# Optimization experiments

Measured on AMD Instinct MI355X. Metric: run time of the kernel, lower is better.

Reference implementation:

```python
import jax, jax.numpy as jnp
import numpy as np

TOP_K = 6
N_EXPERTS = 64
ALPHA = 1e-3


def setup_inputs() -> dict:
    key = jax.random.key(0)
    k1, k2 = jax.random.split(key)
    bsz, seq_len, h = 4, 4096, 2048
    hidden_states = jax.random.normal(k1, (bsz, seq_len, h), dtype=jnp.float32)
    # kaiming_uniform_(a=sqrt(5)) on [E, h] -> bound = 1/sqrt(h)
    bound = 1.0 / np.sqrt(h)
    weight = jax.random.uniform(k2, (N_EXPERTS, h), dtype=jnp.float32, minval=-bound, maxval=bound)
    return {"hidden_states": hidden_states, "weight": weight}


def reference(hidden_states, weight):
    bsz, seq_len, h = hidden_states.shape
    E = weight.shape[0]
    x = hidden_states.reshape(-1, h)                      # [T, h], T = bsz*seq_len
    logits = jnp.einsum('th,eh->te', x, weight)           # router linear (no bias)
    scores = jax.nn.softmax(logits, axis=-1)              # [T, E]
    topk_weight, topk_idx = jax.lax.top_k(scores, TOP_K)  # [T, K]
    # norm_topk_prob renormalization
    topk_weight = topk_weight / (jnp.sum(topk_weight, axis=-1, keepdims=True) + 1e-20)
    # seq_aux auxiliary load-balancing loss (training path)
    idx_b = topk_idx.reshape(bsz, seq_len * TOP_K)        # [B, S*K]
    ce = jnp.sum(jax.nn.one_hot(idx_b, E, dtype=scores.dtype), axis=1)  # [B, E] counts
    ce = ce / (seq_len * TOP_K / E)
    mean_scores = scores.reshape(bsz, seq_len, E).mean(axis=1)          # [B, E]
    aux_loss = jnp.mean(jnp.sum(ce * mean_scores, axis=1)) * ALPHA
    return topk_idx, topk_weight, aux_loss
```

## Files before the change

### kernel.cpp

```cpp
#include <hip/hip_runtime.h>
#include <math.h>

#pragma clang fp contract(off)

typedef float f32x2 __attribute__((ext_vector_type(2)));

#define T_TOKENS 16384
#define HDIM 2048
#define NEXP 64
#define TOPK 6
#define SEQ 4096
#define TPB 32
#define NTHR 256
#define KC 64
#define WS 68
#define LGS 65

__global__ __launch_bounds__(NTHR, 4) void moe_gate_main(
    const float* __restrict__ x, const float* __restrict__ wgt,
    float* __restrict__ out, float* __restrict__ gacc)
{
    __shared__ float w_lds[NEXP * WS];
    __shared__ float lg[TPB * LGS];
    __shared__ float probs[TPB * LGS];
    __shared__ float psum[4 * NEXP];
    __shared__ int   cnt[NEXP];

    const int tid = threadIdx.x;
    const int bid = blockIdx.x;
    const int tb  = bid * TPB;
    const int b   = tb >> 12;

    const int le = tid & 15;
    const int h  = (tid >> 4) & 1;
    const int tg = tid >> 5;
    const int t0 = tg * 4;

    f32x2 acc[4][4];
    #pragma unroll
    for (int je = 0; je < 4; ++je)
        #pragma unroll
        for (int tt = 0; tt < 4; ++tt) { acc[je][tt].x = 0.f; acc[je][tt].y = 0.f; }

    const float* xb = x + (size_t)(tb + t0) * HDIM + 2 * h;

    for (int c = 0; c < HDIM / KC; ++c) {
        const int k0 = c * KC;
        __syncthreads();
        #pragma unroll
        for (int i = 0; i < 4; ++i) {
            int idx = i * NTHR + tid;
            int e = idx >> 4, c4 = idx & 15;
            float4 v = *reinterpret_cast<const float4*>(&wgt[e * HDIM + k0 + c4 * 4]);
            *reinterpret_cast<float4*>(&w_lds[e * WS + c4 * 4]) = v;
        }
        __syncthreads();

        #pragma unroll
        for (int b16 = 0; b16 < 4; ++b16) {
            const int kk = k0 + b16 * 16;
            f32x2 xf[4][4];
            #pragma unroll
            for (int tt = 0; tt < 4; ++tt)
                #pragma unroll
                for (int j = 0; j < 4; ++j)
                    xf[tt][j] = *reinterpret_cast<const f32x2*>(
                        &xb[(size_t)tt * HDIM + kk + 4 * j]);
            #pragma unroll
            for (int j = 3; j >= 0; --j) {
                f32x2 wf[4];
                #pragma unroll
                for (int je = 0; je < 4; ++je)
                    wf[je] = *reinterpret_cast<const f32x2*>(
                        &w_lds[(le + 16 * je) * WS + (kk - k0) + 4 * j + 2 * h]);
                #pragma unroll
                for (int je = 0; je < 4; ++je)
                    #pragma unroll
                    for (int tt = 0; tt < 4; ++tt) {
                        f32x2 p = wf[je] * xf[tt][j];
                        acc[je][tt] = p + acc[je][tt];
                    }
            }
        }
    }

    float* part1 = probs;
    if (h == 1) {
        #pragma unroll
        for (int je = 0; je < 4; ++je)
            #pragma unroll
            for (int tt = 0; tt < 4; ++tt)
                part1[(t0 + tt) * LGS + le + 16 * je] = acc[je][tt].x + acc[je][tt].y;
    }
    if (tid < NEXP) cnt[tid] = 0;
    __syncthreads();
    if (h == 0) {
        #pragma unroll
        for (int je = 0; je < 4; ++je)
            #pragma unroll
            for (int tt = 0; tt < 4; ++tt) {
                float p0 = acc[je][tt].x + acc[je][tt].y;
                lg[(t0 + tt) * LGS + le + 16 * je] =
                    p0 + part1[(t0 + tt) * LGS + le + 16 * je];
            }
    }
    __syncthreads();

    if (tid < TPB) {
        const int t = tid;
        float mx = lg[t * LGS];
        for (int e = 1; e < NEXP; ++e) { float v = lg[t * LGS + e]; if (v > mx) mx = v; }
        for (int e = 0; e < NEXP; ++e)
            probs[t * LGS + e] = expf(lg[t * LGS + e] - mx);
        float r[8];
        #pragma unroll
        for (int j = 0; j < 8; ++j) r[j] = probs[t * LGS + j];
        for (int i = 8; i < 64; i += 8)
            #pragma unroll
            for (int j = 0; j < 8; ++j) r[j] += probs[t * LGS + i + j];
        float S = ((r[0] + r[1]) + (r[2] + r[3])) + ((r[4] + r[5]) + (r[6] + r[7]));
        for (int e = 0; e < NEXP; ++e) probs[t * LGS + e] = probs[t * LGS + e] / S;
    }
    __syncthreads();

    {
        const int e = tid & 63, q = tid >> 6;
        float s = 0.f;
        for (int t = q * 8; t < q * 8 + 8; ++t) s += probs[t * LGS + e];
        psum[q * 64 + e] = s;
    }
    __syncthreads();

    if (tid < TPB) {
        const int t = tid;
        const int gt = tb + t;
        float pv[TOPK]; int pi[TOPK];
        for (int r = 0; r < TOPK; ++r) {
            float bv = -1.f; int be = 0;
            for (int e = 0; e < NEXP; ++e) {
                float v = probs[t * LGS + e];
                if (v > bv) { bv = v; be = e; }
            }
            probs[t * LGS + be] = -1.f;
            pv[r] = bv; pi[r] = be;
            atomicAdd(&cnt[be], 1);
        }
        float wsum = pv[0];
        #pragma unroll
        for (int r = 1; r < TOPK; ++r) wsum += pv[r];
        wsum += 1e-20f;
        #pragma unroll
        for (int r = 0; r < TOPK; ++r) {
            out[(size_t)gt * TOPK + r] = (float)pi[r];
            out[(size_t)T_TOKENS * TOPK + (size_t)gt * TOPK + r] = pv[r] / wsum;
        }
    } else if (tid >= 64 && tid < 128) {
        const int e = tid - 64;
        float s = psum[e] + psum[64 + e] + psum[128 + e] + psum[192 + e];
        atomicAdd(&gacc[b * 64 + e], s);
    }
    __syncthreads();
    if (tid < NEXP) {
        atomicAdd(&gacc[256 + b * 64 + tid], (float)cnt[tid]);
    }
}

__global__ __launch_bounds__(256) void moe_gate_aux(
    const float* __restrict__ gacc, float* __restrict__ out)
{
    __shared__ float red[4];
    const int tid = threadIdx.x;
    float v = gacc[256 + tid] * gacc[tid];
    #pragma unroll
    for (int o = 32; o > 0; o >>= 1) v += __shfl_down(v, o, 64);
    if ((tid & 63) == 0) red[tid >> 6] = v;
    __syncthreads();
    if (tid == 0) {
        float tot = red[0] + red[1] + red[2] + red[3];
        const float scale = (64.0f / (4096.0f * 6.0f)) / 4096.0f;
        out[2 * T_TOKENS * TOPK] = 1e-3f * (tot * scale) * 0.25f;
    }
}

extern "C" void kernel_launch(void* const* d_in, const int* in_sizes, int n_in,
                              void* d_out, int out_size, void* d_ws, size_t ws_size,
                              hipStream_t stream) {
    const float* x   = (const float*)d_in[0];
    const float* wgt = (const float*)d_in[1];
    float* out  = (float*)d_out;
    float* gacc = (float*)d_ws;

    hipMemsetAsync(d_ws, 0, 512 * sizeof(float), stream);
    moe_gate_main<<<T_TOKENS / TPB, NTHR, 0, stream>>>(x, wgt, out, gacc);
    moe_gate_aux<<<1, 256, 0, stream>>>(gacc, out);
}
```

Baseline: 362.9 us.

## Drop LDS weight staging; read weights directly from global with 128-thread blocks

```diff
diff --git a/kernel.cpp b/kernel.cpp
--- a/kernel.cpp
+++ b/kernel.cpp
@@ -2,8 +2,6 @@
 #include <math.h>
 
 #pragma clang fp contract(off)
-
-typedef float f32x2 __attribute__((ext_vector_type(2)));
 
 #define T_TOKENS 16384
 #define HDIM 2048
@@ -11,19 +9,28 @@
 #define TOPK 6
 #define SEQ 4096
 #define TPB 32
-#define NTHR 256
-#define KC 64
-#define WS 68
+#define NTHR 128
 #define LGS 65
 
-__global__ __launch_bounds__(NTHR, 4) void moe_gate_main(
+__device__ __forceinline__ void np_upd(const float4& w0, const float4& w1,
+                                       const float4& w2, const float4& w3,
+                                       const float4& x0, const float4& x1,
+                                       const float4& x2, const float4& x3,
+                                       float acc[4])
+{
+    acc[0] = w0.x*x0.x + (w1.x*x1.x + (w2.x*x2.x + (w3.x*x3.x + acc[0])));
+    acc[1] = w0.y*x0.y + (w1.y*x1.y + (w2.y*x2.y + (w3.y*x3.y + acc[1])));
+    acc[2] = w0.z*x0.z + (w1.z*x1.z + (w2.z*x2.z + (w3.z*x3.z + acc[2])));
+    acc[3] = w0.w*x0.w + (w1.w*x1.w + (w2.w*x2.w + (w3.w*x3.w + acc[3])));
+}
+
+__global__ __launch_bounds__(NTHR, 2) void moe_gate_main(
     const float* __restrict__ x, const float* __restrict__ wgt,
     float* __restrict__ out, float* __restrict__ gacc)
 {
-    __shared__ float w_lds[NEXP * WS];
     __shared__ float lg[TPB * LGS];
     __shared__ float probs[TPB * LGS];
-    __shared__ float psum[4 * NEXP];
+    __shared__ float psum[2 * NEXP];
     __shared__ int   cnt[NEXP];
 
     const int tid = threadIdx.x;
@@ -32,78 +39,81 @@
     const int b   = tb >> 12;
 
     const int le = tid & 15;
-    const int h  = (tid >> 4) & 1;
-    const int tg = tid >> 5;
+    const int tg = tid >> 4;
     const int t0 = tg * 4;
 
-    f32x2 acc[4][4];
+    const float* wp0 = wgt + (size_t)(le     ) * HDIM;
+    const float* wp1 = wgt + (size_t)(le + 16) * HDIM;
+    const float* wp2 = wgt + (size_t)(le + 32) * HDIM;
+    const float* wp3 = wgt + (size_t)(le + 48) * HDIM;
+    const float* xp0 = x + (size_t)(tb + t0    ) * HDIM;
+    const float* xp1 = x + (size_t)(tb + t0 + 1) * HDIM;
+    const float* xp2 = x + (size_t)(tb + t0 + 2) * HDIM;
+    const float* xp3 = x + (size_t)(tb + t0 + 3) * HDIM;
+
+    float acc[4][4][4];
     #pragma unroll
     for (int je = 0; je < 4; ++je)
         #pragma unroll
-        for (int tt = 0; tt < 4; ++tt) { acc[je][tt].x = 0.f; acc[je][tt].y = 0.f; }
-
-    const float* xb = x + (size_t)(tb + t0) * HDIM + 2 * h;
-
-    for (int c = 0; c < HDIM / KC; ++c) {
-        const int k0 = c * KC;
-        __syncthreads();
-        #pragma unroll
-        for (int i = 0; i < 4; ++i) {
-            int idx = i * NTHR + tid;
-            int e = idx >> 4, c4 = idx & 15;
-            float4 v = *reinterpret_cast<const float4*>(&wgt[e * HDIM + k0 + c4 * 4]);
-            *reinterpret_cast<float4*>(&w_lds[e * WS + c4 * 4]) = v;
-        }
-        __syncthreads();
-
-        #pragma unroll
-        for (int b16 = 0; b16 < 4; ++b16) {
-            const int kk = k0 + b16 * 16;
-            f32x2 xf[4][4];
-            #pragma unroll
-            for (int tt = 0; tt < 4; ++tt)
-                #pragma unroll
-                for (int j = 0; j < 4; ++j)
-                    xf[tt][j] = *reinterpret_cast<const f32x2*>(
-                        &xb[(size_t)tt * HDIM + kk + 4 * j]);
-            #pragma unroll
-            for (int j = 3; j >= 0; --j) {
-                f32x2 wf[4];
-                #pragma unroll
-                for (int je = 0; je < 4; ++je)
-                    wf[je] = *reinterpret_cast<const f32x2*>(
-                        &w_lds[(le + 16 * je) * WS + (kk - k0) + 4 * j + 2 * h]);
-                #pragma unroll
-                for (int je = 0; je < 4; ++je)
-                    #pragma unroll
-                    for (int tt = 0; tt < 4; ++tt) {
-                        f32x2 p = wf[je] * xf[tt][j];
-                        acc[je][tt] = p + acc[je][tt];
-                    }
-            }
-        }
-    }
-
-    float* part1 = probs;
-    if (h == 1) {
-        #pragma unroll
-        for (int je = 0; je < 4; ++je)
-            #pragma unroll
-            for (int tt = 0; tt < 4; ++tt)
-                part1[(t0 + tt) * LGS + le + 16 * je] = acc[je][tt].x + acc[je][tt].y;
-    }
+        for (int tt = 0; tt < 4; ++tt)
+            #pragma unroll
+            for (int l = 0; l < 4; ++l) acc[je][tt][l] = 0.f;
+
+    for (int kb = 0; kb < HDIM; kb += 16) {
+        float4 xv[4][4];
+        #pragma unroll
+        for (int j = 0; j < 4; ++j) {
+            xv[0][j] = *reinterpret_cast<const float4*>(xp0 + kb + 4 * j);
+            xv[1][j] = *reinterpret_cast<const float4*>(xp1 + kb + 4 * j);
+            xv[2][j] = *reinterpret_cast<const float4*>(xp2 + kb + 4 * j);
+            xv[3][j] = *reinterpret_cast<const float4*>(xp3 + kb + 4 * j);
+        }
+        {
+            float4 w0 = *reinterpret_cast<const float4*>(wp0 + kb);
+            float4 w1 = *reinterpret_cast<const float4*>(wp0 + kb + 4);
+            float4 w2 = *reinterpret_cast<const float4*>(wp0 + kb + 8);
+            float4 w3 = *reinterpret_cast<const float4*>(wp0 + kb + 12);
+            #pragma unroll
+            for (int tt = 0; tt < 4; ++tt)
+                np_upd(w0, w1, w2, w3, xv[tt][0], xv[tt][1], xv[tt][2], xv[tt][3], acc[0][tt]);
+        }
+        {
+            float4 w0 = *reinterpret_cast<const float4*>(wp1 + kb);
+            float4 w1 = *reinterpret_cast<const float4*>(wp1 + kb + 4);
+            float4 w2 = *reinterpret_cast<const float4*>(wp1 + kb + 8);
+            float4 w3 = *reinterpret_cast<const float4*>(wp1 + kb + 12);
+            #pragma unroll
+            for (int tt = 0; tt < 4; ++tt)
+                np_upd(w0, w1, w2, w3, xv[tt][0], xv[tt][1], xv[tt][2], xv[tt][3], acc[1][tt]);
+        }
+        {
+            float4 w0 = *reinterpret_cast<const float4*>(wp2 + kb);
+            float4 w1 = *reinterpret_cast<const float4*>(wp2 + kb + 4);
+            float4 w2 = *reinterpret_cast<const float4*>(wp2 + kb + 8);
+            float4 w3 = *reinterpret_cast<const float4*>(wp2 + kb + 12);
+            #pragma unroll
+            for (int tt = 0; tt < 4; ++tt)
+                np_upd(w0, w1, w2, w3, xv[tt][0], xv[tt][1], xv[tt][2], xv[tt][3], acc[2][tt]);
+        }
+        {
+            float4 w0 = *reinterpret_cast<const float4*>(wp3 + kb);
+            float4 w1 = *reinterpret_cast<const float4*>(wp3 + kb + 4);
+            float4 w2 = *reinterpret_cast<const float4*>(wp3 + kb + 8);
+            float4 w3 = *reinterpret_cast<const float4*>(wp3 + kb + 12);
+            #pragma unroll
+            for (int tt = 0; tt < 4; ++tt)
+                np_upd(w0, w1, w2, w3, xv[tt][0], xv[tt][1], xv[tt][2], xv[tt][3], acc[3][tt]);
+        }
+    }
+
+    #pragma unroll
+    for (int je = 0; je < 4; ++je)
+        #pragma unroll
+        for (int tt = 0; tt < 4; ++tt) {
+            float v = (acc[je][tt][0] + acc[je][tt][1]) + (acc[je][tt][2] + acc[je][tt][3]);
+            lg[(t0 + tt) * LGS + le + 16 * je] = v;
+        }
     if (tid < NEXP) cnt[tid] = 0;
-    __syncthreads();
-    if (h == 0) {
-        #pragma unroll
-        for (int je = 0; je < 4; ++je)
-            #pragma unroll
-            for (int tt = 0; tt < 4; ++tt) {
-                float p0 = acc[je][tt].x + acc[je][tt].y;
-                lg[(t0 + tt) * LGS + le + 16 * je] =
-                    p0 + part1[(t0 + tt) * LGS + le + 16 * je];
-            }
-    }
     __syncthreads();
 
     if (tid < TPB) {
@@ -126,7 +136,7 @@
     {
         const int e = tid & 63, q = tid >> 6;
         float s = 0.f;
-        for (int t = q * 8; t < q * 8 + 8; ++t) s += probs[t * LGS + e];
+        for (int t = q * 16; t < q * 16 + 16; ++t) s += probs[t * LGS + e];
         psum[q * 64 + e] = s;
     }
     __syncthreads();
@@ -156,8 +166,7 @@
         }
     } else if (tid >= 64 && tid < 128) {
         const int e = tid - 64;
-        float s = psum[e] + psum[64 + e] + psum[128 + e] + psum[192 + e];
-        atomicAdd(&gacc[b * 64 + e], s);
+        atomicAdd(&gacc[b * 64 + e], psum[e] + psum[64 + e]);
     }
     __syncthreads();
     if (tid < NEXP) {
```

Measured after the change: 573.5 us. 58.1% more time.
